# Performance work log

Hardware: AMD Instinct MI355X
Metric: run time of the kernel (lower is better)

## Reference

```python
import jax, jax.numpy as jnp
import numpy as np

BASE_MARGIN = 0.1
N = 8192


def setup_inputs() -> dict:
    key = jax.random.key(0)
    k1, k2, k3 = jax.random.split(key, 3)
    predictions = jax.random.normal(k1, (N,), dtype=jnp.float32)
    targets = jax.random.normal(k2, (N,), dtype=jnp.float32)
    uncertainties = jax.random.uniform(k3, (N,), dtype=jnp.float32)
    return {"predictions": predictions, "targets": targets, "uncertainties": uncertainties}


def reference(predictions, targets, uncertainties):
    n = predictions.shape[0]
    # pairwise differences, [n, n]; entry (i, j) corresponds to pair (i, j)
    tdiff = targets[:, None] - targets[None, :]
    pdiff = predictions[:, None] - predictions[None, :]
    # adaptive margin: base_margin * clamp(|t_i - t_j|, 0.1, 1.0)
    margin = BASE_MARGIN * jnp.clip(jnp.abs(tdiff), 0.1, 1.0)
    # uncertainty weight: 1 / (1 + u_i + u_j)
    weight = 1.0 / (1.0 + uncertainties[:, None] + uncertainties[None, :])
    # if t_i > t_j: hinge(p_j - p_i + margin) = hinge(-pdiff + margin)
    # if t_j > t_i: hinge(p_i - p_j + margin) = hinge(+pdiff + margin)
    sgn = jnp.sign(tdiff)
    hinge = jnp.maximum(-sgn * pdiff + margin, 0.0)
    # only upper-triangular pairs (i < j) with t_i != t_j contribute
    iu = jnp.triu(jnp.ones((n, n), dtype=bool), k=1)
    mask = iu & (tdiff != 0.0)
    loss = jnp.sum(jnp.where(mask, weight * hinge, 0.0))
    count = jnp.sum(mask)
    return loss / jnp.maximum(count, 1).astype(loss.dtype)
```

## Files before the change

kernel.cpp:

```cpp
#include <hip/hip_runtime.h>


constexpr int CH  = 64;
constexpr int WPB = 4;

__device__ __forceinline__ float bcastf(float v, int lane) {
    return __int_as_float(__builtin_amdgcn_readlane(__float_as_int(v), lane));
}

template<bool DIAG, bool EDGE>
__device__ __forceinline__ void chunk64(
    float pi, float ti, float ui1, bool ivalid,
    float tjv, float pjv, float ujv,
    int i, int j0, int n,
    float& acc, unsigned& cnt)
{
    #pragma unroll
    for (int jj = 0; jj < CH; ++jj) {
        const float tj = bcastf(tjv, jj);
        const float pj = bcastf(pjv, jj);
        const float uj = bcastf(ujv, jj);
        const float tdiff = ti - tj;
        const float pdiff = pi - pj;
        const float m3 = __builtin_amdgcn_fmed3f(fabsf(tdiff), 0.1f, 1.0f);
        const float spd = __uint_as_float(__float_as_uint(pdiff) ^
                                          (__float_as_uint(tdiff) & 0x80000000u));
        const float h = fmaxf(fmaf(m3, 0.1f, -spd), 0.0f);
        const float w = __builtin_amdgcn_rcpf(ui1 + uj);
        bool use = (tdiff != 0.0f);
        if (DIAG) use = use && ((j0 + jj) > i);
        if (EDGE) use = use && ivalid && ((j0 + jj) < n);
        acc = fmaf(use ? w : 0.0f, h, acc);
        cnt += (unsigned)__popcll(__ballot(use));
    }
}

__global__ __launch_bounds__(CH * WPB) void arl_pair_kernel(
    const float* __restrict__ pred, const float* __restrict__ targ,
    const float* __restrict__ unc, int n, int nc, int nTiles,
    float2* __restrict__ partials)
{
    const int tid    = threadIdx.x;
    const int lane   = tid & 63;
    const int wid    = tid >> 6;
    const int tileId = blockIdx.x * WPB + wid;

    float acc = 0.0f;
    unsigned cnt = 0;

    if (tileId < nTiles) {
        const float nch = (float)nc + 0.5f;
        int r = (int)(nch - sqrtf(nch * nch - 2.0f * (float)tileId));
        if (r < 0) r = 0;
        if (r > nc - 1) r = nc - 1;
        auto base = [nc](int rr) { return rr * nc - (rr * (rr - 1)) / 2; };
        while (r + 1 < nc && base(r + 1) <= tileId) ++r;
        while (r > 0 && base(r) > tileId) --r;
        const int c = r + (tileId - base(r));

        const int i0 = r * CH, j0 = c * CH;
        const int i  = i0 + lane;
        const int jg = j0 + lane;
        const bool full = (i0 + CH <= n) && (j0 + CH <= n);

        if (full) {
            const float pi  = pred[i];
            const float ti  = targ[i];
            const float ui1 = 1.0f + unc[i];
            const float tjv = targ[jg];
            const float pjv = pred[jg];
            const float ujv = unc[jg];
            if (r == c) chunk64<true , false>(pi, ti, ui1, true, tjv, pjv, ujv, i, j0, n, acc, cnt);
            else        chunk64<false, false>(pi, ti, ui1, true, tjv, pjv, ujv, i, j0, n, acc, cnt);
        } else {
            const bool iv = i < n, jv = jg < n;
            const float pi  = iv ? pred[i] : 0.0f;
            const float ti  = iv ? targ[i] : 0.0f;
            const float ui1 = 1.0f + (iv ? unc[i] : 0.0f);
            const float tjv = jv ? targ[jg] : 0.0f;
            const float pjv = jv ? pred[jg] : 0.0f;
            const float ujv = jv ? unc[jg] : 0.0f;
            if (r == c) chunk64<true , true >(pi, ti, ui1, iv, tjv, pjv, ujv, i, j0, n, acc, cnt);
            else        chunk64<false, true >(pi, ti, ui1, iv, tjv, pjv, ujv, i, j0, n, acc, cnt);
        }
    }

    for (int off = 32; off > 0; off >>= 1) acc += __shfl_down(acc, off);

    __shared__ float sa[WPB], sc[WPB];
    if (lane == 0) { sa[wid] = acc; sc[wid] = (float)cnt; }
    __syncthreads();
    if (tid == 0) {
        float a2 = 0.0f, c2 = 0.0f;
        #pragma unroll
        for (int w = 0; w < WPB; ++w) { a2 += sa[w]; c2 += sc[w]; }
        partials[blockIdx.x] = float2{a2, c2};
    }
}

__global__ __launch_bounds__(256) void arl_finalize(
    const float2* __restrict__ partials, int nPartials, float* __restrict__ out)
{
    float a = 0.0f, c = 0.0f;
    for (int k = threadIdx.x; k < nPartials; k += 256) {
        const float2 v = partials[k];
        a += v.x; c += v.y;
    }
    for (int off = 32; off > 0; off >>= 1) {
        a += __shfl_down(a, off);
        c += __shfl_down(c, off);
    }
    __shared__ float sa[4], sc[4];
    const int lane = threadIdx.x & 63, wid = threadIdx.x >> 6;
    if (lane == 0) { sa[wid] = a; sc[wid] = c; }
    __syncthreads();
    if (threadIdx.x == 0) {
        double A = 0.0, C = 0.0;
        #pragma unroll
        for (int w = 0; w < 4; ++w) { A += (double)sa[w]; C += (double)sc[w]; }
        out[0] = (float)(A / (C > 0.0 ? C : 1.0));
    }
}

extern "C" void kernel_launch(void* const* d_in, const int* in_sizes, int n_in,
                              void* d_out, int out_size, void* d_ws, size_t ws_size,
                              hipStream_t stream) {
    const float* pred = (const float*)d_in[0];
    const float* targ = (const float*)d_in[1];
    const float* unc  = (const float*)d_in[2];
    const int n = in_sizes[0];

    const int nc     = (n + CH - 1) / CH;
    const int nTiles = nc * (nc + 1) / 2;
    const int nBlocks = (nTiles + WPB - 1) / WPB;

    float2* partials = (float2*)d_ws;

    arl_pair_kernel<<<nBlocks, CH * WPB, 0, stream>>>(pred, targ, unc, n, nc,
                                                      nTiles, partials);
    arl_finalize<<<1, 256, 0, stream>>>(partials, nBlocks, (float*)d_out);
}
```

Before: 77.67 us.

## Fuse pair and finalize kernels via cooperative launch with grid-stride tiles

Merges the pairwise tile kernel and the finalize reduction into one cooperative kernel that uses grid.sync before block 0 reduces the partials. The work becomes a persistent grid of 256 blocks of 1024 threads, each wave looping over triangular tiles with a grid stride, which removes the second launch and per-block overhead. In exchange it adds a grid-wide barrier, requires cooperative launch residency, and large blocks may hurt occupancy or load balance.

```diff
diff --git a/kernel.cpp b/kernel.cpp
--- a/kernel.cpp
+++ b/kernel.cpp
@@ -1,8 +1,10 @@
 #include <hip/hip_runtime.h>
+#include <hip/hip_cooperative_groups.h>
+
+namespace cg = cooperative_groups;
 
 
-constexpr int CH  = 64;
-constexpr int WPB = 4;
+constexpr int CH = 64;
 
 __device__ __forceinline__ float bcastf(float v, int lane) {
     return __int_as_float(__builtin_amdgcn_readlane(__float_as_int(v), lane));
@@ -35,22 +37,26 @@
     }
 }
 
-__global__ __launch_bounds__(CH * WPB) void arl_pair_kernel(
+__global__ __launch_bounds__(1024) void arl_fused(
     const float* __restrict__ pred, const float* __restrict__ targ,
     const float* __restrict__ unc, int n, int nc, int nTiles,
-    float2* __restrict__ partials)
+    float2* __restrict__ partials, float* __restrict__ out)
 {
-    const int tid    = threadIdx.x;
-    const int lane   = tid & 63;
-    const int wid    = tid >> 6;
-    const int tileId = blockIdx.x * WPB + wid;
+    cg::grid_group grid = cg::this_grid();
+
+    const int tid  = threadIdx.x;
+    const int lane = tid & 63;
+    const int wid  = tid >> 6;
+    const int wpb  = blockDim.x >> 6;
+    const int gwid = blockIdx.x * wpb + wid;
+    const int nw   = gridDim.x * wpb;
 
     float acc = 0.0f;
     unsigned cnt = 0;
 
-    if (tileId < nTiles) {
+    for (int tileId = gwid; tileId < nTiles; tileId += nw) {
         const float nch = (float)nc + 0.5f;
-        int r = (int)(nch - sqrtf(nch * nch - 2.0f * (float)tileId));
+        int r = (int)(nch - sqrtf(fmaxf(nch * nch - 2.0f * (float)tileId, 0.0f)));
         if (r < 0) r = 0;
         if (r > nc - 1) r = nc - 1;
         auto base = [nc](int rr) { return rr * nc - (rr * (rr - 1)) / 2; };
@@ -87,38 +93,35 @@
 
     for (int off = 32; off > 0; off >>= 1) acc += __shfl_down(acc, off);
 
-    __shared__ float sa[WPB], sc[WPB];
+    __shared__ float sa[16], sc[16];
     if (lane == 0) { sa[wid] = acc; sc[wid] = (float)cnt; }
     __syncthreads();
     if (tid == 0) {
         float a2 = 0.0f, c2 = 0.0f;
-        #pragma unroll
-        for (int w = 0; w < WPB; ++w) { a2 += sa[w]; c2 += sc[w]; }
+        for (int w = 0; w < wpb; ++w) { a2 += sa[w]; c2 += sc[w]; }
         partials[blockIdx.x] = float2{a2, c2};
     }
-}
 
-__global__ __launch_bounds__(256) void arl_finalize(
-    const float2* __restrict__ partials, int nPartials, float* __restrict__ out)
-{
-    float a = 0.0f, c = 0.0f;
-    for (int k = threadIdx.x; k < nPartials; k += 256) {
-        const float2 v = partials[k];
-        a += v.x; c += v.y;
-    }
-    for (int off = 32; off > 0; off >>= 1) {
-        a += __shfl_down(a, off);
-        c += __shfl_down(c, off);
-    }
-    __shared__ float sa[4], sc[4];
-    const int lane = threadIdx.x & 63, wid = threadIdx.x >> 6;
-    if (lane == 0) { sa[wid] = a; sc[wid] = c; }
-    __syncthreads();
-    if (threadIdx.x == 0) {
-        double A = 0.0, C = 0.0;
-        #pragma unroll
-        for (int w = 0; w < 4; ++w) { A += (double)sa[w]; C += (double)sc[w]; }
-        out[0] = (float)(A / (C > 0.0 ? C : 1.0));
+    grid.sync();
+
+    if (blockIdx.x == 0) {
+        float a = 0.0f, c = 0.0f;
+        for (int k = tid; k < (int)gridDim.x; k += blockDim.x) {
+            const float2 v = partials[k];
+            a += v.x; c += v.y;
+        }
+        for (int off = 32; off > 0; off >>= 1) {
+            a += __shfl_down(a, off);
+            c += __shfl_down(c, off);
+        }
+        __syncthreads();
+        if (lane == 0) { sa[wid] = a; sc[wid] = c; }
+        __syncthreads();
+        if (tid == 0) {
+            double A = 0.0, C = 0.0;
+            for (int w = 0; w < wpb; ++w) { A += (double)sa[w]; C += (double)sc[w]; }
+            out[0] = (float)(A / (C > 0.0 ? C : 1.0));
+        }
     }
 }
 
@@ -128,15 +131,18 @@
     const float* pred = (const float*)d_in[0];
     const float* targ = (const float*)d_in[1];
     const float* unc  = (const float*)d_in[2];
-    const int n = in_sizes[0];
+    int n = in_sizes[0];
 
-    const int nc     = (n + CH - 1) / CH;
-    const int nTiles = nc * (nc + 1) / 2;
-    const int nBlocks = (nTiles + WPB - 1) / WPB;
+    int nc     = (n + CH - 1) / CH;
+    int nTiles = nc * (nc + 1) / 2;
+    float2* partials = (float2*)d_ws;
+    float* out = (float*)d_out;
 
-    float2* partials = (float2*)d_ws;
+    dim3 gridDim(256);
+    dim3 blockDim(1024);
 
-    arl_pair_kernel<<<nBlocks, CH * WPB, 0, stream>>>(pred, targ, unc, n, nc,
-                                                      nTiles, partials);
-    arl_finalize<<<1, 256, 0, stream>>>(partials, nBlocks, (float*)d_out);
+    void* args[] = { (void*)&pred, (void*)&targ, (void*)&unc,
+                     (void*)&n, (void*)&nc, (void*)&nTiles,
+                     (void*)&partials, (void*)&out };
+    hipLaunchCooperativeKernel((void*)arl_fused, gridDim, blockDim, args, 0, stream);
 }
```

New measurement: 113.5 us. +46.2%, slower.

## Compute four i-rows per lane to reuse broadcast j values across a taller tile

Applied to the files above, without the earlier changes.

Each wavefront now covers 256 i-rows by 64 j-columns, and each lane handles four i values. Every readlane broadcast of a j element is therefore shared by four pair computations instead of one. The triangular tile indexing is rewritten for the non-square tile shape, and diagonal and edge handling uses a per-row offset test. This cuts the broadcast overhead per pair and the number of tiles, at the cost of more registers and a partial unroll of the j loop.

```diff
diff --git a/kernel.cpp b/kernel.cpp
--- a/kernel.cpp
+++ b/kernel.cpp
@@ -2,42 +2,30 @@
 
 
 constexpr int CH  = 64;
+constexpr int IR  = 4;
 constexpr int WPB = 4;
 
 __device__ __forceinline__ float bcastf(float v, int lane) {
     return __int_as_float(__builtin_amdgcn_readlane(__float_as_int(v), lane));
 }
 
-template<bool DIAG, bool EDGE>
-__device__ __forceinline__ void chunk64(
-    float pi, float ti, float ui1, bool ivalid,
-    float tjv, float pjv, float ujv,
-    int i, int j0, int n,
-    float& acc, unsigned& cnt)
+__device__ __forceinline__ void pair_math(
+    float pi, float ti, float ui1, float tj, float pj, float uj,
+    float& h_out, float& w_out, bool& nz_out)
 {
-    #pragma unroll
-    for (int jj = 0; jj < CH; ++jj) {
-        const float tj = bcastf(tjv, jj);
-        const float pj = bcastf(pjv, jj);
-        const float uj = bcastf(ujv, jj);
-        const float tdiff = ti - tj;
-        const float pdiff = pi - pj;
-        const float m3 = __builtin_amdgcn_fmed3f(fabsf(tdiff), 0.1f, 1.0f);
-        const float spd = __uint_as_float(__float_as_uint(pdiff) ^
-                                          (__float_as_uint(tdiff) & 0x80000000u));
-        const float h = fmaxf(fmaf(m3, 0.1f, -spd), 0.0f);
-        const float w = __builtin_amdgcn_rcpf(ui1 + uj);
-        bool use = (tdiff != 0.0f);
-        if (DIAG) use = use && ((j0 + jj) > i);
-        if (EDGE) use = use && ivalid && ((j0 + jj) < n);
-        acc = fmaf(use ? w : 0.0f, h, acc);
-        cnt += (unsigned)__popcll(__ballot(use));
-    }
+    const float tdiff = ti - tj;
+    const float pdiff = pi - pj;
+    const float m3 = __builtin_amdgcn_fmed3f(fabsf(tdiff), 0.1f, 1.0f);
+    const float spd = __uint_as_float(__float_as_uint(pdiff) ^
+                                      (__float_as_uint(tdiff) & 0x80000000u));
+    h_out  = fmaxf(fmaf(m3, 0.1f, -spd), 0.0f);
+    w_out  = __builtin_amdgcn_rcpf(ui1 + uj);
+    nz_out = (tdiff != 0.0f);
 }
 
 __global__ __launch_bounds__(CH * WPB) void arl_pair_kernel(
     const float* __restrict__ pred, const float* __restrict__ targ,
-    const float* __restrict__ unc, int n, int nc, int nTiles,
+    const float* __restrict__ unc, int n, int ncj, int nti, int nTiles,
     float2* __restrict__ partials)
 {
     const int tid    = threadIdx.x;
@@ -45,50 +33,93 @@
     const int wid    = tid >> 6;
     const int tileId = blockIdx.x * WPB + wid;
 
-    float acc = 0.0f;
+    float acc[IR] = {0.f, 0.f, 0.f, 0.f};
     unsigned cnt = 0;
 
     if (tileId < nTiles) {
-        const float nch = (float)nc + 0.5f;
-        int r = (int)(nch - sqrtf(nch * nch - 2.0f * (float)tileId));
-        if (r < 0) r = 0;
-        if (r > nc - 1) r = nc - 1;
-        auto base = [nc](int rr) { return rr * nc - (rr * (rr - 1)) / 2; };
-        while (r + 1 < nc && base(r + 1) <= tileId) ++r;
-        while (r > 0 && base(r) > tileId) --r;
-        const int c = r + (tileId - base(r));
+        const float A = (float)ncj + 2.0f;
+        int it = (int)((A - sqrtf(fmaxf(A * A - 8.0f * (float)tileId, 0.0f))) * 0.25f);
+        if (it < 0) it = 0;
+        if (it > nti - 1) it = nti - 1;
+        auto base = [ncj](int r) { return r * ncj - 2 * r * (r - 1); };
+        while (it + 1 < nti && base(it + 1) <= tileId) ++it;
+        while (it > 0 && base(it) > tileId) --it;
+        const int jt = 4 * it + (tileId - base(it));
 
-        const int i0 = r * CH, j0 = c * CH;
-        const int i  = i0 + lane;
+        const int i0 = it * (CH * IR);
+        const int j0 = jt * CH;
         const int jg = j0 + lane;
-        const bool full = (i0 + CH <= n) && (j0 + CH <= n);
 
-        if (full) {
-            const float pi  = pred[i];
-            const float ti  = targ[i];
-            const float ui1 = 1.0f + unc[i];
+        const bool hot = (jt >= 4 * it + IR) && (i0 + CH * IR <= n) && (j0 + CH <= n);
+
+        if (hot) {
+            float pi[IR], ti[IR], ui1[IR];
+            #pragma unroll
+            for (int k = 0; k < IR; ++k) {
+                const int i = i0 + CH * k + lane;
+                pi[k]  = pred[i];
+                ti[k]  = targ[i];
+                ui1[k] = 1.0f + unc[i];
+            }
             const float tjv = targ[jg];
             const float pjv = pred[jg];
             const float ujv = unc[jg];
-            if (r == c) chunk64<true , false>(pi, ti, ui1, true, tjv, pjv, ujv, i, j0, n, acc, cnt);
-            else        chunk64<false, false>(pi, ti, ui1, true, tjv, pjv, ujv, i, j0, n, acc, cnt);
+
+            #pragma unroll 8
+            for (int jj = 0; jj < CH; ++jj) {
+                const float tj = bcastf(tjv, jj);
+                const float pj = bcastf(pjv, jj);
+                const float uj = bcastf(ujv, jj);
+                #pragma unroll
+                for (int k = 0; k < IR; ++k) {
+                    float h, w; bool nz;
+                    pair_math(pi[k], ti[k], ui1[k], tj, pj, uj, h, w, nz);
+                    acc[k] = fmaf(nz ? w : 0.0f, h, acc[k]);
+                    cnt += (unsigned)__popcll(__ballot(nz));
+                }
+            }
         } else {
-            const bool iv = i < n, jv = jg < n;
-            const float pi  = iv ? pred[i] : 0.0f;
-            const float ti  = iv ? targ[i] : 0.0f;
-            const float ui1 = 1.0f + (iv ? unc[i] : 0.0f);
+            int   dk[IR];
+            bool  iv[IR];
+            float pi[IR], ti[IR], ui1[IR];
+            #pragma unroll
+            for (int k = 0; k < IR; ++k) {
+                const int i = i0 + CH * k + lane;
+                dk[k] = jt - 4 * it - k;
+                iv[k] = i < n;
+                pi[k]  = iv[k] ? pred[i] : 0.0f;
+                ti[k]  = iv[k] ? targ[i] : 0.0f;
+                ui1[k] = 1.0f + (iv[k] ? unc[i] : 0.0f);
+            }
+            const bool jv = jg < n;
             const float tjv = jv ? targ[jg] : 0.0f;
             const float pjv = jv ? pred[jg] : 0.0f;
             const float ujv = jv ? unc[jg] : 0.0f;
-            if (r == c) chunk64<true , true >(pi, ti, ui1, iv, tjv, pjv, ujv, i, j0, n, acc, cnt);
-            else        chunk64<false, true >(pi, ti, ui1, iv, tjv, pjv, ujv, i, j0, n, acc, cnt);
+
+            #pragma unroll 4
+            for (int jj = 0; jj < CH; ++jj) {
+                const bool jok = (j0 + jj) < n;
+                const float tj = bcastf(tjv, jj);
+                const float pj = bcastf(pjv, jj);
+                const float uj = bcastf(ujv, jj);
+                #pragma unroll
+                for (int k = 0; k < IR; ++k) {
+                    float h, w; bool nz;
+                    pair_math(pi[k], ti[k], ui1[k], tj, pj, uj, h, w, nz);
+                    const bool pos = (dk[k] > 0) || (dk[k] == 0 && lane < jj);
+                    const bool use = nz && pos && iv[k] && jok;
+                    acc[k] = fmaf(use ? w : 0.0f, h, acc[k]);
+                    cnt += (unsigned)__popcll(__ballot(use));
+                }
+            }
         }
     }
 
-    for (int off = 32; off > 0; off >>= 1) acc += __shfl_down(acc, off);
+    float acct = (acc[0] + acc[1]) + (acc[2] + acc[3]);
+    for (int off = 32; off > 0; off >>= 1) acct += __shfl_down(acct, off);
 
     __shared__ float sa[WPB], sc[WPB];
-    if (lane == 0) { sa[wid] = acc; sc[wid] = (float)cnt; }
+    if (lane == 0) { sa[wid] = acct; sc[wid] = (float)cnt; }
     __syncthreads();
     if (tid == 0) {
         float a2 = 0.0f, c2 = 0.0f;
@@ -130,13 +161,14 @@
     const float* unc  = (const float*)d_in[2];
     const int n = in_sizes[0];
 
-    const int nc     = (n + CH - 1) / CH;
-    const int nTiles = nc * (nc + 1) / 2;
+    const int nti = (n + CH * IR - 1) / (CH * IR);
+    const int ncj = (n + CH - 1) / CH;
+    const int nTiles  = nti * ncj - 2 * nti * (nti - 1);
     const int nBlocks = (nTiles + WPB - 1) / WPB;
 
     float2* partials = (float2*)d_ws;
 
-    arl_pair_kernel<<<nBlocks, CH * WPB, 0, stream>>>(pred, targ, unc, n, nc,
-                                                      nTiles, partials);
+    arl_pair_kernel<<<nBlocks, CH * WPB, 0, stream>>>(pred, targ, unc, n, ncj,
+                                                      nti, nTiles, partials);
     arl_finalize<<<1, 256, 0, stream>>>(partials, nBlocks, (float*)d_out);
 }
```

After: 82.85 us. +6.7%, slower.
